# Kernel tuning notes

Measured on AMD Instinct MI355X. Metric: run time of the kernel, lower is better.

Reference implementation:

```python
import jax, jax.numpy as jnp
import numpy as np

H = 64  # hidden_size hardcoded in the module


def setup_inputs() -> dict:
    key = jax.random.key(0)
    ks = jax.random.split(key, 8)
    B, T, I, O = 4096, 256, 128, 10
    s_ih = 1.0 / np.sqrt(H)
    return {
        "x": jax.random.normal(ks[0], (B, T, I), dtype=jnp.float32),
        # PyTorch LSTM params, gate order (i, f, g, o)
        "W_ih": jax.random.uniform(ks[1], (4 * H, I), minval=-s_ih, maxval=s_ih, dtype=jnp.float32),
        "W_hh": jax.random.uniform(ks[2], (4 * H, H), minval=-s_ih, maxval=s_ih, dtype=jnp.float32),
        "b_ih": jax.random.uniform(ks[3], (4 * H,), minval=-s_ih, maxval=s_ih, dtype=jnp.float32),
        "b_hh": jax.random.uniform(ks[4], (4 * H,), minval=-s_ih, maxval=s_ih, dtype=jnp.float32),
        "W_out": jax.random.uniform(ks[5], (O, H), minval=-s_ih, maxval=s_ih, dtype=jnp.float32),
        "b_out": jax.random.uniform(ks[6], (O,), minval=-s_ih, maxval=s_ih, dtype=jnp.float32),
    }


def _lstm_last_h(x, W_ih, W_hh, b_ih, b_hh):
    B, T, I = x.shape
    # Precompute input contributions for all timesteps: [T, B, 4H]
    gx = jnp.einsum('bti,gi->tbg', x, W_ih) + (b_ih + b_hh)

    def step(carry, g_t):
        h, c = carry
        g = g_t + h @ W_hh.T  # [B, 4H]
        i = jax.nn.sigmoid(g[:, 0 * H:1 * H])
        f = jax.nn.sigmoid(g[:, 1 * H:2 * H])
        gg = jnp.tanh(g[:, 2 * H:3 * H])
        o = jax.nn.sigmoid(g[:, 3 * H:4 * H])
        c = f * c + i * gg
        h = o * jnp.tanh(c)
        return (h, c), None

    h0 = jnp.zeros((B, H), dtype=x.dtype)
    c0 = jnp.zeros((B, H), dtype=x.dtype)
    (h_last, _), _ = jax.lax.scan(step, (h0, c0), gx)
    return h_last


def reference(x, W_ih, W_hh, b_ih, b_hh, W_out, b_out):
    # forward reshapes x to [B, T, I]; our x is already that shape.
    h_last = _lstm_last_h(x, W_ih, W_hh, b_ih, b_hh)  # r_out[:, -1, :]
    return h_last @ W_out.T + b_out
```

## Files before the change

kernel.cpp:

```cpp
#include <hip/hip_runtime.h>


typedef __attribute__((ext_vector_type(8))) short bf16x8;
typedef __attribute__((ext_vector_type(4))) float f32x4;
typedef __attribute__((ext_vector_type(2))) unsigned u32x2;

#define T_STEPS 256
#define L2E 1.44269504f

#define XF_OFF 0
#define H_OFF  16384
#define HF_OFF 20480
#define LDS_SZ 24576

__device__ __forceinline__ short f2bf(float f) {
    unsigned u = __float_as_uint(f);
    u += 0x7FFFu + ((u >> 16) & 1u);
    return (short)(u >> 16);
}
__device__ __forceinline__ unsigned cvt_pk(float lo, float hi) {
    unsigned r;
    asm("v_cvt_pk_bf16_f32 %0, %1, %2" : "=v"(r) : "v"(lo), "v"(hi));
    return r;
}
__device__ __forceinline__ float frcp(float x) { float r; asm("v_rcp_f32 %0, %1" : "=v"(r) : "v"(x)); return r; }
__device__ __forceinline__ float fexp2(float x) { float r; asm("v_exp_f32 %0, %1" : "=v"(r) : "v"(x)); return r; }

#define MF(A, Bf, C) (C) = __builtin_amdgcn_mfma_f32_16x16x32_bf16((A), (Bf), (C), 0, 0, 0)
#define SYNC { asm volatile("s_waitcnt lgkmcnt(0)" ::: "memory"); __builtin_amdgcn_s_barrier(); }

__global__ __launch_bounds__(256, 1) void lstm_kernel(
    const float* __restrict__ x,
    const float* __restrict__ W_ih,
    const float* __restrict__ W_hh,
    const float* __restrict__ b_ih,
    const float* __restrict__ b_hh,
    const float* __restrict__ W_out,
    const float* __restrict__ b_out,
    float* __restrict__ out)
{
    __shared__ __align__(16) char smem[LDS_SZ];

    const int tid  = threadIdx.x;
    const int lane = tid & 63;
    const int q    = tid >> 6;
    const int l15  = lane & 15;
    const int l4   = lane >> 4;
    const int b0   = blockIdx.x * 16;

    bf16x8 Bih[4][4];
    bf16x8 Bhh[4][2];
    f32x4  biasC[4];
#pragma unroll
    for (int nt = 0; nt < 4; ++nt) {
        const float scl = (nt == 2) ? (2.0f * L2E) : (-L2E);
        const int row = nt * 64 + q * 16 + l15;
#pragma unroll
        for (int ks = 0; ks < 4; ++ks) {
            const float* p = W_ih + row * 128 + ks * 32 + l4 * 8;
            f32x4 a = *(const f32x4*)p;
            f32x4 b = *(const f32x4*)(p + 4);
            bf16x8 wv;
#pragma unroll
            for (int j = 0; j < 4; ++j) { wv[j] = f2bf(a[j] * scl); wv[4 + j] = f2bf(b[j] * scl); }
            Bih[nt][ks] = wv;
        }
#pragma unroll
        for (int ks = 0; ks < 2; ++ks) {
            const float* p = W_hh + row * 64 + ks * 32 + l4 * 8;
            f32x4 a = *(const f32x4*)p;
            f32x4 b = *(const f32x4*)(p + 4);
            bf16x8 wv;
#pragma unroll
            for (int j = 0; j < 4; ++j) { wv[j] = f2bf(a[j] * scl); wv[4 + j] = f2bf(b[j] * scl); }
            Bhh[nt][ks] = wv;
        }
        const float bb = (b_ih[row] + b_hh[row]) * scl;
        biasC[nt] = (f32x4){bb, bb, bb, bb};
    }

    int xf_rd[4];
#pragma unroll
    for (int ks = 0; ks < 4; ++ks)
        xf_rd[ks] = (((ks * 64 + lane) * 16) ^ ((ks & 3) << 6));

    const int jcol = q * 16 + l15;
    int hb_wr[4];
#pragma unroll
    for (int r = 0; r < 4; ++r) {
        const int b = l4 * 4 + r;
        hb_wr[r] = ((b * 128 + jcol * 2) ^ ((b & 7) << 4) ^ ((b >> 3) << 5));
    }
    int hb_rd[2];
#pragma unroll
    for (int ks = 0; ks < 2; ++ks)
        hb_rd[ks] = ((l15 * 128 + ks * 64 + l4 * 16) ^ ((l15 & 7) << 4) ^ ((l15 >> 3) << 5));

    const int srow = tid >> 5;
    const int scc  = tid & 31;
    const int sks  = scc >> 3;
    const int sl4  = (scc & 7) >> 1;
    const int sh   = scc & 1;
    const int xf_wr0 = (((sks * 64 + sl4 * 16 + srow) * 16 + sh * 8) ^ ((sks & 3) << 6));
    const int xf_wr1 = (((sks * 64 + sl4 * 16 + srow + 8) * 16 + sh * 8) ^ ((sks & 3) << 6));
    const float* xsrc0 = x + (size_t)(b0 + srow) * (T_STEPS * 128) + scc * 4;
    const float* xsrc1 = x + (size_t)(b0 + srow + 8) * (T_STEPS * 128) + scc * 4;

#pragma unroll
    for (int s = 0; s < 3; ++s) {
        f32x4 v0 = *(const f32x4*)(xsrc0 + (size_t)s * 128);
        f32x4 v1 = *(const f32x4*)(xsrc1 + (size_t)s * 128);
        u32x2 wv0; wv0.x = cvt_pk(v0[0], v0[1]); wv0.y = cvt_pk(v0[2], v0[3]);
        u32x2 wv1; wv1.x = cvt_pk(v1[0], v1[1]); wv1.y = cvt_pk(v1[2], v1[3]);
        *(u32x2*)(smem + XF_OFF + s * 4096 + xf_wr0) = wv0;
        *(u32x2*)(smem + XF_OFF + s * 4096 + xf_wr1) = wv1;
    }
    f32x4 P0[4], P1[4];
#pragma unroll
    for (int s = 0; s < 4; ++s) {
        P0[s] = *(const f32x4*)(xsrc0 + (size_t)(s + 3) * 128);
        P1[s] = *(const f32x4*)(xsrc1 + (size_t)(s + 3) * 128);
    }
    ((unsigned long long*)(smem + H_OFF + 2048))[tid] = 0ull;

    SYNC;

    float c[4]  = {0.f, 0.f, 0.f, 0.f};
    float hl[4] = {0.f, 0.f, 0.f, 0.f};

    f32x4 accA[4], accB[4];
    {
        bf16x8 Ax0 = *(const bf16x8*)(smem + XF_OFF + xf_rd[0]);
        bf16x8 Ax1 = *(const bf16x8*)(smem + XF_OFF + xf_rd[1]);
        bf16x8 Ax2 = *(const bf16x8*)(smem + XF_OFF + xf_rd[2]);
        bf16x8 Ax3 = *(const bf16x8*)(smem + XF_OFF + xf_rd[3]);
        accA[0] = biasC[0]; accA[1] = biasC[1]; accA[2] = biasC[2]; accA[3] = biasC[3];
        MF(Ax0, Bih[0][0], accA[0]); MF(Ax0, Bih[1][0], accA[1]);
        MF(Ax0, Bih[2][0], accA[2]); MF(Ax0, Bih[3][0], accA[3]);
        MF(Ax1, Bih[0][1], accA[0]); MF(Ax1, Bih[1][1], accA[1]);
        MF(Ax1, Bih[2][1], accA[2]); MF(Ax1, Bih[3][1], accA[3]);
        MF(Ax2, Bih[0][2], accA[0]); MF(Ax2, Bih[1][2], accA[1]);
        MF(Ax2, Bih[2][2], accA[2]); MF(Ax2, Bih[3][2], accA[3]);
        MF(Ax3, Bih[0][3], accA[0]); MF(Ax3, Bih[1][3], accA[1]);
        MF(Ax3, Bih[2][3], accA[2]); MF(Ax3, Bih[3][3], accA[3]);
    }

#define WINDOW(tt, T4, ACUR, ANXT)                                             \
  {                                                                            \
    const char* hbR = smem + H_OFF + ((((T4) & 1) ^ 1) * 2048);                \
    char*       hbW = smem + H_OFF + (((T4) & 1) * 2048);                      \
    const char* xfb = smem + XF_OFF + ((((T4) + 1) & 3) * 4096);               \
    char*       xfw = smem + XF_OFF + ((((T4) + 3) & 3) * 4096);               \
    bf16x8 Ax0 = *(const bf16x8*)(xfb + xf_rd[0]);                             \
    bf16x8 Ax1 = *(const bf16x8*)(xfb + xf_rd[1]);                             \
    bf16x8 Ax2 = *(const bf16x8*)(xfb + xf_rd[2]);                             \
    bf16x8 Ax3 = *(const bf16x8*)(xfb + xf_rd[3]);                             \
    bf16x8 Ah0 = *(const bf16x8*)(hbR + hb_rd[0]);                             \
    bf16x8 Ah1 = *(const bf16x8*)(hbR + hb_rd[1]);                             \
    ANXT[0] = biasC[0]; ANXT[1] = biasC[1];                                    \
    ANXT[2] = biasC[2]; ANXT[3] = biasC[3];                                    \
    MF(Ax0, Bih[0][0], ANXT[0]); MF(Ax0, Bih[1][0], ANXT[1]);                  \
    MF(Ax0, Bih[2][0], ANXT[2]); MF(Ax0, Bih[3][0], ANXT[3]);                  \
    MF(Ax1, Bih[0][1], ANXT[0]); MF(Ax1, Bih[1][1], ANXT[1]);                  \
    MF(Ax1, Bih[2][1], ANXT[2]); MF(Ax1, Bih[3][1], ANXT[3]);                  \
    MF(Ax2, Bih[0][2], ANXT[0]); MF(Ax2, Bih[1][2], ANXT[1]);                  \
    MF(Ax2, Bih[2][2], ANXT[2]); MF(Ax2, Bih[3][2], ANXT[3]);                  \
    MF(Ax3, Bih[0][3], ANXT[0]); MF(Ax3, Bih[1][3], ANXT[1]);                  \
    MF(Ax3, Bih[2][3], ANXT[2]); MF(Ax3, Bih[3][3], ANXT[3]);                  \
    MF(Ah0, Bhh[0][0], ACUR[0]); MF(Ah0, Bhh[1][0], ACUR[1]);                  \
    MF(Ah0, Bhh[2][0], ACUR[2]); MF(Ah0, Bhh[3][0], ACUR[3]);                  \
    MF(Ah1, Bhh[0][1], ACUR[0]); MF(Ah1, Bhh[1][1], ACUR[1]);                  \
    MF(Ah1, Bhh[2][1], ACUR[2]); MF(Ah1, Bhh[3][1], ACUR[3]);                  \
    {                                                                          \
      u32x2 wv0; wv0.x = cvt_pk(P0[(T4)][0], P0[(T4)][1]);                     \
      wv0.y = cvt_pk(P0[(T4)][2], P0[(T4)][3]);                                \
      u32x2 wv1; wv1.x = cvt_pk(P1[(T4)][0], P1[(T4)][1]);                     \
      wv1.y = cvt_pk(P1[(T4)][2], P1[(T4)][3]);                                \
      *(u32x2*)(xfw + xf_wr0) = wv0;                                           \
      *(u32x2*)(xfw + xf_wr1) = wv1;                                           \
      const int tc = ((tt) + 7) & 255;                                         \
      P0[(T4)] = *(const f32x4*)(xsrc0 + (size_t)tc * 128);                    \
      P1[(T4)] = *(const f32x4*)(xsrc1 + (size_t)tc * 128);                    \
    }                                                                          \
    _Pragma("unroll")                                                          \
    for (int r = 0; r < 4; ++r) {                                              \
      float Ei = fexp2(ACUR[0][r]);                              \
      float Ef = fexp2(ACUR[1][r]);                              \
      float Eg = fexp2(ACUR[2][r]);                             \
      float Eo = fexp2(ACUR[3][r]);                              \
      float u  = 1.0f + Ei;                                                    \
      float v  = Eg + 1.0f;                                                    \
      float w  = 1.0f + Ef;                                                    \
      float uv = u * v;                                                        \
      float num = __builtin_fmaf(c[r], uv, (Eg - 1.0f) * w);                   \
      float cc  = num * frcp(uv * w);                                          \
      c[r] = cc;                                                               \
      float E2 = fexp2(cc * (2.0f * L2E));                                     \
      hl[r] = (E2 - 1.0f) * frcp((E2 + 1.0f) * (1.0f + Eo));                   \
    }                                                                          \
    {                                                                          \
      unsigned w01 = cvt_pk(hl[0], hl[1]);                                     \
      unsigned w23 = cvt_pk(hl[2], hl[3]);                                     \
      *(short*)(hbW + hb_wr[0]) = (short)w01;                                  \
      *(short*)(hbW + hb_wr[1]) = (short)(w01 >> 16);                          \
      *(short*)(hbW + hb_wr[2]) = (short)w23;                                  \
      *(short*)(hbW + hb_wr[3]) = (short)(w23 >> 16);                          \
    }                                                                          \
    SYNC;                                                                      \
  }

    for (int t = 0; t < T_STEPS; t += 4) {
        WINDOW(t,     0, accA, accB);
        WINDOW(t + 1, 1, accB, accA);
        WINDOW(t + 2, 2, accA, accB);
        WINDOW(t + 3, 3, accB, accA);
    }
#undef WINDOW

#pragma unroll
    for (int r = 0; r < 4; ++r) {
        const int b = l4 * 4 + r;
        *(float*)(smem + HF_OFF + (b * 64 + jcol) * 4) = hl[r];
    }
    SYNC;

    if (tid < 160) {
        const int b = tid / 10;
        const int o = tid - b * 10;
        const f32x4* hf = (const f32x4*)(smem + HF_OFF + b * 256);
        const f32x4* wr = (const f32x4*)(W_out + o * 64);
        float s = b_out[o];
#pragma unroll
        for (int j4 = 0; j4 < 16; ++j4) {
            f32x4 h4 = hf[j4];
            f32x4 w4 = wr[j4];
            s += h4[0] * w4[0] + h4[1] * w4[1] + h4[2] * w4[2] + h4[3] * w4[3];
        }
        out[(b0 + b) * 10 + o] = s;
    }
}

extern "C" void kernel_launch(void* const* d_in, const int* in_sizes, int n_in,
                              void* d_out, int out_size, void* d_ws, size_t ws_size,
                              hipStream_t stream) {
    const float* x     = (const float*)d_in[0];
    const float* W_ih  = (const float*)d_in[1];
    const float* W_hh  = (const float*)d_in[2];
    const float* b_ih  = (const float*)d_in[3];
    const float* b_hh  = (const float*)d_in[4];
    const float* W_out = (const float*)d_in[5];
    const float* b_out = (const float*)d_in[6];
    (void)in_sizes; (void)n_in; (void)out_size; (void)d_ws; (void)ws_size;

    lstm_kernel<<<dim3(256), dim3(256), 0, stream>>>(
        x, W_ih, W_hh, b_ih, b_hh, W_out, b_out, (float*)d_out);
}
```

Measured before the change: 166.3 us.

## Deepen input-projection pipeline to two steps and interleave MFMAs with gate math

Keeps four accumulator sets so the input-projection GEMM runs two timesteps ahead. It places those MFMAs between the gate exponentials and the cell update, and splits the elementwise math into phases. The goal is to hide MFMA and transcendental latency on the serial recurrence path. It costs extra accumulator registers, which may reduce occupancy or cause spills.

```diff
diff --git a/kernel.cpp b/kernel.cpp
--- a/kernel.cpp
+++ b/kernel.cpp
@@ -128,49 +128,59 @@
     float c[4]  = {0.f, 0.f, 0.f, 0.f};
     float hl[4] = {0.f, 0.f, 0.f, 0.f};
 
-    f32x4 accA[4], accB[4];
-    {
-        bf16x8 Ax0 = *(const bf16x8*)(smem + XF_OFF + xf_rd[0]);
-        bf16x8 Ax1 = *(const bf16x8*)(smem + XF_OFF + xf_rd[1]);
-        bf16x8 Ax2 = *(const bf16x8*)(smem + XF_OFF + xf_rd[2]);
-        bf16x8 Ax3 = *(const bf16x8*)(smem + XF_OFF + xf_rd[3]);
-        accA[0] = biasC[0]; accA[1] = biasC[1]; accA[2] = biasC[2]; accA[3] = biasC[3];
-        MF(Ax0, Bih[0][0], accA[0]); MF(Ax0, Bih[1][0], accA[1]);
-        MF(Ax0, Bih[2][0], accA[2]); MF(Ax0, Bih[3][0], accA[3]);
-        MF(Ax1, Bih[0][1], accA[0]); MF(Ax1, Bih[1][1], accA[1]);
-        MF(Ax1, Bih[2][1], accA[2]); MF(Ax1, Bih[3][1], accA[3]);
-        MF(Ax2, Bih[0][2], accA[0]); MF(Ax2, Bih[1][2], accA[1]);
-        MF(Ax2, Bih[2][2], accA[2]); MF(Ax2, Bih[3][2], accA[3]);
-        MF(Ax3, Bih[0][3], accA[0]); MF(Ax3, Bih[1][3], accA[1]);
-        MF(Ax3, Bih[2][3], accA[2]); MF(Ax3, Bih[3][3], accA[3]);
-    }
-
-#define WINDOW(tt, T4, ACUR, ANXT)                                             \
+    f32x4 acc[4][4];
+
+#define XGEMM(SET, SLOT)                                                       \
+    {                                                                          \
+        const char* xfb_ = smem + XF_OFF + (SLOT) * 4096;                      \
+        bf16x8 Ax0 = *(const bf16x8*)(xfb_ + xf_rd[0]);                        \
+        bf16x8 Ax1 = *(const bf16x8*)(xfb_ + xf_rd[1]);                        \
+        bf16x8 Ax2 = *(const bf16x8*)(xfb_ + xf_rd[2]);                        \
+        bf16x8 Ax3 = *(const bf16x8*)(xfb_ + xf_rd[3]);                        \
+        acc[SET][0] = biasC[0]; acc[SET][1] = biasC[1];                        \
+        acc[SET][2] = biasC[2]; acc[SET][3] = biasC[3];                        \
+        MF(Ax0, Bih[0][0], acc[SET][0]); MF(Ax0, Bih[1][0], acc[SET][1]);      \
+        MF(Ax0, Bih[2][0], acc[SET][2]); MF(Ax0, Bih[3][0], acc[SET][3]);      \
+        MF(Ax1, Bih[0][1], acc[SET][0]); MF(Ax1, Bih[1][1], acc[SET][1]);      \
+        MF(Ax1, Bih[2][1], acc[SET][2]); MF(Ax1, Bih[3][1], acc[SET][3]);      \
+        MF(Ax2, Bih[0][2], acc[SET][0]); MF(Ax2, Bih[1][2], acc[SET][1]);      \
+        MF(Ax2, Bih[2][2], acc[SET][2]); MF(Ax2, Bih[3][2], acc[SET][3]);      \
+        MF(Ax3, Bih[0][3], acc[SET][0]); MF(Ax3, Bih[1][3], acc[SET][1]);      \
+        MF(Ax3, Bih[2][3], acc[SET][2]); MF(Ax3, Bih[3][3], acc[SET][3]);      \
+    }
+
+    XGEMM(0, 0);
+    XGEMM(1, 1);
+
+#define WINDOW(tt, T4)                                                         \
   {                                                                            \
     const char* hbR = smem + H_OFF + ((((T4) & 1) ^ 1) * 2048);                \
     char*       hbW = smem + H_OFF + (((T4) & 1) * 2048);                      \
-    const char* xfb = smem + XF_OFF + ((((T4) + 1) & 3) * 4096);               \
     char*       xfw = smem + XF_OFF + ((((T4) + 3) & 3) * 4096);               \
-    bf16x8 Ax0 = *(const bf16x8*)(xfb + xf_rd[0]);                             \
-    bf16x8 Ax1 = *(const bf16x8*)(xfb + xf_rd[1]);                             \
-    bf16x8 Ax2 = *(const bf16x8*)(xfb + xf_rd[2]);                             \
-    bf16x8 Ax3 = *(const bf16x8*)(xfb + xf_rd[3]);                             \
     bf16x8 Ah0 = *(const bf16x8*)(hbR + hb_rd[0]);                             \
     bf16x8 Ah1 = *(const bf16x8*)(hbR + hb_rd[1]);                             \
-    ANXT[0] = biasC[0]; ANXT[1] = biasC[1];                                    \
-    ANXT[2] = biasC[2]; ANXT[3] = biasC[3];                                    \
-    MF(Ax0, Bih[0][0], ANXT[0]); MF(Ax0, Bih[1][0], ANXT[1]);                  \
-    MF(Ax0, Bih[2][0], ANXT[2]); MF(Ax0, Bih[3][0], ANXT[3]);                  \
-    MF(Ax1, Bih[0][1], ANXT[0]); MF(Ax1, Bih[1][1], ANXT[1]);                  \
-    MF(Ax1, Bih[2][1], ANXT[2]); MF(Ax1, Bih[3][1], ANXT[3]);                  \
-    MF(Ax2, Bih[0][2], ANXT[0]); MF(Ax2, Bih[1][2], ANXT[1]);                  \
-    MF(Ax2, Bih[2][2], ANXT[2]); MF(Ax2, Bih[3][2], ANXT[3]);                  \
-    MF(Ax3, Bih[0][3], ANXT[0]); MF(Ax3, Bih[1][3], ANXT[1]);                  \
-    MF(Ax3, Bih[2][3], ANXT[2]); MF(Ax3, Bih[3][3], ANXT[3]);                  \
-    MF(Ah0, Bhh[0][0], ACUR[0]); MF(Ah0, Bhh[1][0], ACUR[1]);                  \
-    MF(Ah0, Bhh[2][0], ACUR[2]); MF(Ah0, Bhh[3][0], ACUR[3]);                  \
-    MF(Ah1, Bhh[0][1], ACUR[0]); MF(Ah1, Bhh[1][1], ACUR[1]);                  \
-    MF(Ah1, Bhh[2][1], ACUR[2]); MF(Ah1, Bhh[3][1], ACUR[3]);                  \
+    MF(Ah0, Bhh[0][0], acc[T4][0]); MF(Ah0, Bhh[1][0], acc[T4][1]);            \
+    MF(Ah0, Bhh[2][0], acc[T4][2]); MF(Ah0, Bhh[3][0], acc[T4][3]);            \
+    MF(Ah1, Bhh[0][1], acc[T4][0]); MF(Ah1, Bhh[1][1], acc[T4][1]);            \
+    MF(Ah1, Bhh[2][1], acc[T4][2]); MF(Ah1, Bhh[3][1], acc[T4][3]);            \
+    float Ei[4], Ef[4], Eg[4], Eo[4], E2[4];                                   \
+    _Pragma("unroll")                                                          \
+    for (int r = 0; r < 4; ++r) {                                              \
+      Ei[r] = fexp2(acc[T4][0][r]);                                            \
+      Ef[r] = fexp2(acc[T4][1][r]);                                            \
+      Eg[r] = fexp2(acc[T4][2][r]);                                            \
+      Eo[r] = fexp2(acc[T4][3][r]);                                            \
+    }                                                                          \
+    XGEMM((((T4) + 2) & 3), (((T4) + 2) & 3));                                 \
+    _Pragma("unroll")                                                          \
+    for (int r = 0; r < 4; ++r) {                                              \
+      float u  = 1.0f + Ei[r];                                                 \
+      float v  = Eg[r] + 1.0f;                                                 \
+      float w  = 1.0f + Ef[r];                                                 \
+      float uv = u * v;                                                        \
+      float num = __builtin_fmaf(c[r], uv, (Eg[r] - 1.0f) * w);                \
+      c[r] = num * frcp(uv * w);                                               \
+    }                                                                          \
     {                                                                          \
       u32x2 wv0; wv0.x = cvt_pk(P0[(T4)][0], P0[(T4)][1]);                     \
       wv0.y = cvt_pk(P0[(T4)][2], P0[(T4)][3]);                                \
@@ -178,26 +188,18 @@
       wv1.y = cvt_pk(P1[(T4)][2], P1[(T4)][3]);                                \
       *(u32x2*)(xfw + xf_wr0) = wv0;                                           \
       *(u32x2*)(xfw + xf_wr1) = wv1;                                           \
+    }                                                                          \
+    _Pragma("unroll")                                                          \
+    for (int r = 0; r < 4; ++r)                                                \
+      E2[r] = fexp2(c[r] * (2.0f * L2E));                                      \
+    {                                                                          \
       const int tc = ((tt) + 7) & 255;                                         \
       P0[(T4)] = *(const f32x4*)(xsrc0 + (size_t)tc * 128);                    \
       P1[(T4)] = *(const f32x4*)(xsrc1 + (size_t)tc * 128);                    \
     }                                                                          \
     _Pragma("unroll")                                                          \
-    for (int r = 0; r < 4; ++r) {                                              \
-      float Ei = fexp2(ACUR[0][r]);                              \
-      float Ef = fexp2(ACUR[1][r]);                              \
-      float Eg = fexp2(ACUR[2][r]);                             \
-      float Eo = fexp2(ACUR[3][r]);                              \
-      float u  = 1.0f + Ei;                                                    \
-      float v  = Eg + 1.0f;                                                    \
-      float w  = 1.0f + Ef;                                                    \
-      float uv = u * v;                                                        \
-      float num = __builtin_fmaf(c[r], uv, (Eg - 1.0f) * w);                   \
-      float cc  = num * frcp(uv * w);                                          \
-      c[r] = cc;                                                               \
-      float E2 = fexp2(cc * (2.0f * L2E));                                     \
-      hl[r] = (E2 - 1.0f) * frcp((E2 + 1.0f) * (1.0f + Eo));                   \
-    }                                                                          \
+    for (int r = 0; r < 4; ++r)                                                \
+      hl[r] = (E2[r] - 1.0f) * frcp((E2[r] + 1.0f) * (1.0f + Eo[r]));          \
     {                                                                          \
       unsigned w01 = cvt_pk(hl[0], hl[1]);                                     \
       unsigned w23 = cvt_pk(hl[2], hl[3]);                                     \
@@ -210,12 +212,13 @@
   }
 
     for (int t = 0; t < T_STEPS; t += 4) {
-        WINDOW(t,     0, accA, accB);
-        WINDOW(t + 1, 1, accB, accA);
-        WINDOW(t + 2, 2, accA, accB);
-        WINDOW(t + 3, 3, accB, accA);
+        WINDOW(t,     0);
+        WINDOW(t + 1, 1);
+        WINDOW(t + 2, 2);
+        WINDOW(t + 3, 3);
     }
 #undef WINDOW
+#undef XGEMM
 
 #pragma unroll
     for (int r = 0; r < 4; ++r) {
```

After: 163.6 us, median of 2. No clear change (-1.6%).
